# Performance work log

Hardware: AMD Instinct MI355X
Metric: run time of the kernel (lower is better)

The kernel has to match this reference:

```python
import jax, jax.numpy as jnp
import numpy as np

OUT_H, OUT_W = 7, 7
SPATIAL_SCALE = 0.0625
N_IMG, C, H, W = 2, 256, 38, 38
NUM_ROIS = 256
IMG_MAX = 607.9  # keeps floor(coord*scale) <= 37


def setup_inputs() -> dict:
    key = jax.random.key(0)
    k_feat, k_b, k_xa, k_xb, k_ya, k_yb = jax.random.split(key, 6)
    feat = jax.random.normal(k_feat, (N_IMG, C, H, W), dtype=jnp.float32)
    bidx = jax.random.randint(k_b, (NUM_ROIS,), 0, N_IMG).astype(jnp.float32)
    xa = jax.random.uniform(k_xa, (NUM_ROIS,), minval=0.0, maxval=IMG_MAX)
    xb = jax.random.uniform(k_xb, (NUM_ROIS,), minval=0.0, maxval=IMG_MAX)
    ya = jax.random.uniform(k_ya, (NUM_ROIS,), minval=0.0, maxval=IMG_MAX)
    yb = jax.random.uniform(k_yb, (NUM_ROIS,), minval=0.0, maxval=IMG_MAX)
    rois = jnp.stack([bidx,
                      jnp.minimum(xa, xb), jnp.minimum(ya, yb),
                      jnp.maximum(xa, xb), jnp.maximum(ya, yb)], axis=1)
    return {"input": feat, "rois": rois.astype(jnp.float32)}


def _roi_max_pool(feat_all, rois):
    # feat_all: (N, C, H, W); rois: (R, 5) = (batch_idx, x1, y1, x2, y2)
    H_, W_ = feat_all.shape[2], feat_all.shape[3]
    b = rois[:, 0].astype(jnp.int32)
    # torch: rois[:,1:].mul_(scale); rois.long() -> truncation (== floor for >=0)
    coords = jnp.floor(rois[:, 1:] * SPATIAL_SCALE).astype(jnp.int32)
    x1, y1, x2, y2 = coords[:, 0], coords[:, 1], coords[:, 2], coords[:, 3]
    rh = y2 - y1 + 1  # inclusive crop: [y1, y2+1)
    rw = x2 - x1 + 1
    feat = feat_all[b]  # (R, C, H, W) per-ROI gather of its image
    neg = jnp.array(-jnp.inf, feat.dtype)

    # separable adaptive max pool: rows then cols
    hs = jnp.arange(H_)
    rows = []
    for i in range(OUT_H):  # fixed small loop over output bins
        hstart = y1 + (i * rh) // OUT_H                       # floor(i*rh/OUT_H)
        hend = y1 + ((i + 1) * rh + OUT_H - 1) // OUT_H       # ceil
        m = (hs[None, :] >= hstart[:, None]) & (hs[None, :] < hend[:, None])  # (R,H)
        rows.append(jnp.max(jnp.where(m[:, None, :, None], feat, neg), axis=2))  # (R,C,W)
    rowmax = jnp.stack(rows, axis=2)  # (R, C, OUT_H, W)

    ws = jnp.arange(W_)
    cols = []
    for j in range(OUT_W):
        wstart = x1 + (j * rw) // OUT_W
        wend = x1 + ((j + 1) * rw + OUT_W - 1) // OUT_W
        m = (ws[None, :] >= wstart[:, None]) & (ws[None, :] < wend[:, None])  # (R,W)
        cols.append(jnp.max(jnp.where(m[:, None, None, :], rowmax, neg), axis=3))  # (R,C,OUT_H)
    return jnp.stack(cols, axis=3)  # (R, C, OUT_H, OUT_W)


def reference(input, rois):
    return _roi_max_pool(input, rois)
```

## Files before the change

### kernel.cpp

```cpp
#include <hip/hip_runtime.h>
#include <math.h>

#define OUT_H 7
#define OUT_W 7
#define N_C 256
#define FH 38
#define FW 38
#define NUM_ROIS 256
#define SPATIAL_SCALE 0.0625f
#define PLANE (FH * FW)

#define CC 8
#define CHUNKS (N_C / CC)

__global__ __launch_bounds__(266) void roi_pool_kernel(
    const float* __restrict__ feat,
    const float* __restrict__ rois,
    float* __restrict__ out)
{
    __shared__ float rowmax[CC][OUT_H][FW];

    int blk   = blockIdx.x;
    int r     = blk / CHUNKS;
    int chunk = blk - r * CHUNKS;
    int c0    = chunk * CC;

    const float* roi = rois + r * 5;
    int b  = __builtin_amdgcn_readfirstlane((int)roi[0]);
    int x1 = __builtin_amdgcn_readfirstlane((int)(roi[1] * SPATIAL_SCALE));
    int y1 = __builtin_amdgcn_readfirstlane((int)(roi[2] * SPATIAL_SCALE));
    int x2 = __builtin_amdgcn_readfirstlane((int)(roi[3] * SPATIAL_SCALE));
    int y2 = __builtin_amdgcn_readfirstlane((int)(roi[4] * SPATIAL_SCALE));
    int rh = y2 - y1 + 1;
    int rw = x2 - x1 + 1;

    int w = threadIdx.x;
    int i = threadIdx.y;

    int hstart = y1 + (i * rh) / OUT_H;
    int hend   = y1 + ((i + 1) * rh + OUT_H - 1) / OUT_H;

    const float* fcol = feat + ((size_t)b * N_C + c0) * PLANE + w;

    float m[CC];
    #pragma unroll
    for (int cl = 0; cl < CC; ++cl) m[cl] = -INFINITY;

    for (int h = hstart; h < hend; ++h) {
        int off = h * FW;
        #pragma unroll
        for (int cl = 0; cl < CC; ++cl)
            m[cl] = fmaxf(m[cl], fcol[off + cl * PLANE]);
    }

    #pragma unroll
    for (int cl = 0; cl < CC; ++cl)
        rowmax[cl][i][w] = m[cl];

    __syncthreads();

    int t = threadIdx.y * FW + threadIdx.x;
    float* obase = out + ((size_t)r * N_C + c0) * (OUT_H * OUT_W);
    for (int task = t; task < CC * OUT_H * OUT_W; task += 266) {
        int cl  = task / (OUT_H * OUT_W);
        int pos = task - cl * (OUT_H * OUT_W);
        int oi  = pos / OUT_W;
        int j   = pos - oi * OUT_W;
        int wstart = x1 + (j * rw) / OUT_W;
        int wend   = x1 + ((j + 1) * rw + OUT_W - 1) / OUT_W;
        float mm = -INFINITY;
        for (int ww = wstart; ww < wend; ++ww)
            mm = fmaxf(mm, rowmax[cl][oi][ww]);
        obase[task] = mm;
    }
}

extern "C" void kernel_launch(void* const* d_in, const int* in_sizes, int n_in,
                              void* d_out, int out_size, void* d_ws, size_t ws_size,
                              hipStream_t stream) {
    const float* feat = (const float*)d_in[0];
    const float* rois = (const float*)d_in[1];
    float* out = (float*)d_out;

    dim3 block(FW, OUT_H);
    int  grid = NUM_ROIS * CHUNKS;
    roi_pool_kernel<<<grid, block, 0, stream>>>(feat, rois, out);
}
```

Measured before the change: 77.91 us.

## Vectorize row loads with float2 and double channels per block

Each thread now loads two adjacent columns with float2 instead of one float, and the block gains a z dimension to cover 16 channels per block instead of 8, which halves the grid. Column bin bounds are computed once into shared memory, and the second stage gives each thread four channels for one fixed output position. The goal is fewer memory instructions and less per-block overhead, at the cost of more registers per thread and fewer blocks to spread across CUs.

```diff
diff --git a/kernel.cpp b/kernel.cpp
--- a/kernel.cpp
+++ b/kernel.cpp
@@ -10,7 +10,7 @@
 #define SPATIAL_SCALE 0.0625f
 #define PLANE (FH * FW)
 
-#define CC 8
+#define CC 16
 #define CHUNKS (N_C / CC)
 
 __global__ __launch_bounds__(266) void roi_pool_kernel(
@@ -19,6 +19,7 @@
     float* __restrict__ out)
 {
     __shared__ float rowmax[CC][OUT_H][FW];
+    __shared__ int wse[2][OUT_W];
 
     int blk   = blockIdx.x;
     int r     = blk / CHUNKS;
@@ -34,44 +35,59 @@
     int rh = y2 - y1 + 1;
     int rw = x2 - x1 + 1;
 
-    int w = threadIdx.x;
-    int i = threadIdx.y;
+    int tx = threadIdx.x;
+    int ty = threadIdx.y;
+    int tz = threadIdx.z;
+    int lin = tx + 19 * (ty + 7 * tz);
 
+    if (lin < OUT_W) {
+        int j = lin;
+        wse[0][j] = x1 + (j * rw) / OUT_W;
+        wse[1][j] = x1 + ((j + 1) * rw + OUT_W - 1) / OUT_W;
+    }
+
+    int i = ty;
     int hstart = y1 + (i * rh) / OUT_H;
     int hend   = y1 + ((i + 1) * rh + OUT_H - 1) / OUT_H;
 
-    const float* fcol = feat + ((size_t)b * N_C + c0) * PLANE + w;
+    const float* pbase = feat + ((size_t)b * N_C + c0 + tz * 8) * PLANE;
+    int off = hstart * FW + 2 * tx;
 
-    float m[CC];
+    float2 m[8];
     #pragma unroll
-    for (int cl = 0; cl < CC; ++cl) m[cl] = -INFINITY;
+    for (int cl = 0; cl < 8; ++cl) { m[cl].x = -INFINITY; m[cl].y = -INFINITY; }
 
-    for (int h = hstart; h < hend; ++h) {
-        int off = h * FW;
+    for (int h = hstart; h < hend; ++h, off += FW) {
         #pragma unroll
-        for (int cl = 0; cl < CC; ++cl)
-            m[cl] = fmaxf(m[cl], fcol[off + cl * PLANE]);
+        for (int cl = 0; cl < 8; ++cl) {
+            float2 v = *(const float2*)&pbase[cl * PLANE + off];
+            m[cl].x = fmaxf(m[cl].x, v.x);
+            m[cl].y = fmaxf(m[cl].y, v.y);
+        }
     }
 
     #pragma unroll
-    for (int cl = 0; cl < CC; ++cl)
-        rowmax[cl][i][w] = m[cl];
+    for (int cl = 0; cl < 8; ++cl)
+        *(float2*)&rowmax[tz * 8 + cl][i][2 * tx] = m[cl];
 
     __syncthreads();
 
-    int t = threadIdx.y * FW + threadIdx.x;
-    float* obase = out + ((size_t)r * N_C + c0) * (OUT_H * OUT_W);
-    for (int task = t; task < CC * OUT_H * OUT_W; task += 266) {
-        int cl  = task / (OUT_H * OUT_W);
-        int pos = task - cl * (OUT_H * OUT_W);
+    if (lin < 196) {
+        int g   = lin / 49;
+        int pos = lin - g * 49;
         int oi  = pos / OUT_W;
         int j   = pos - oi * OUT_W;
-        int wstart = x1 + (j * rw) / OUT_W;
-        int wend   = x1 + ((j + 1) * rw + OUT_W - 1) / OUT_W;
-        float mm = -INFINITY;
-        for (int ww = wstart; ww < wend; ++ww)
-            mm = fmaxf(mm, rowmax[cl][oi][ww]);
-        obase[task] = mm;
+        int wstart = wse[0][j];
+        int wend   = wse[1][j];
+        float* obase = out + ((size_t)r * N_C + c0) * (OUT_H * OUT_W);
+        #pragma unroll
+        for (int q = 0; q < 4; ++q) {
+            int cl = g * 4 + q;
+            float mm = -INFINITY;
+            for (int ww = wstart; ww < wend; ++ww)
+                mm = fmaxf(mm, rowmax[cl][oi][ww]);
+            obase[cl * (OUT_H * OUT_W) + pos] = mm;
+        }
     }
 }
 
@@ -82,7 +98,7 @@
     const float* rois = (const float*)d_in[1];
     float* out = (float*)d_out;
 
-    dim3 block(FW, OUT_H);
+    dim3 block(19, OUT_H, 2);
     int  grid = NUM_ROIS * CHUNKS;
     roi_pool_kernel<<<grid, block, 0, stream>>>(feat, rois, out);
 }
```

New measurement: 78.01 us, median of 2. No clear change (+0.1%).
